# Performance work log

Measured on AMD Instinct MI355X. Metric: run time of the kernel, lower is better.

Reference implementation:

```python
import jax, jax.numpy as jnp
import numpy as np

Y_SCALE = 0.01  # fixed weight quantization scale (q_scale of the int8 weights)


def setup_inputs() -> dict:
    key = jax.random.key(0)
    kx, kw, kb = jax.random.split(key, 3)
    B, S, IN, OUT = 4, 2048, 4096, 4096
    x = jax.random.normal(kx, (B, S, IN), dtype=jnp.float32)
    # int8 quantized weights, stored transposed as (in_features, out_features)
    weight_q = jax.random.randint(kw, (IN, OUT), -128, 128, dtype=jnp.int32)
    bias = jax.random.normal(kb, (OUT,), dtype=jnp.float32)
    return {"x": x, "weight_q": weight_q, "bias": bias}


def reference(x, weight_q, bias):
    # Per-batch-sample dynamic activation scale: max(|x_i|)/128 over each [S, IN] slice
    x_scale = jnp.max(jnp.abs(x), axis=(1, 2), keepdims=True) / 128.0  # [B,1,1]
    # int8 quantize: round + clip
    xq = jnp.clip(jnp.round(x / x_scale), -128, 127).astype(jnp.int8)  # [B,S,IN]
    wq = weight_q.astype(jnp.int8)                                      # [IN,OUT]
    c = jax.lax.dot_general(
        xq, wq,
        dimension_numbers=(((2,), (0,)), ((), ())),
        preferred_element_type=jnp.int32,
    )  # [B,S,OUT]
    # dequantize and bias-add
    y = c.astype(jnp.float32) * (x_scale * Y_SCALE)
    return y + bias
```

## Files before the change

### kernel.cpp

```cpp
#include <hip/hip_runtime.h>
#include <stdint.h>

#define K_DIM 4096
#define N_DIM 4096
#define M_DIM 8192
#define S_ROWS 2048
#define NT 32

typedef int v4i __attribute__((ext_vector_type(4)));

__device__ __forceinline__ void gload16(const void* g, void* l) {
    __builtin_amdgcn_global_load_lds(
        (const __attribute__((address_space(1))) unsigned int*)g,
        (__attribute__((address_space(3))) unsigned int*)l, 16, 0, 0);
}

__device__ __forceinline__ void barrier() {
    asm volatile("" ::: "memory");
    __builtin_amdgcn_s_barrier();
    asm volatile("" ::: "memory");
}

__global__ void absmax_kernel(const float* __restrict__ x, unsigned* __restrict__ amax) {
    int b = blockIdx.y;
    const float4* xb = (const float4*)(x + (size_t)b * S_ROWS * K_DIM);
    int tid = blockIdx.x * 256 + threadIdx.x;
    const int stride = 1024 * 256;
    float m = 0.f;
#pragma unroll
    for (int i = 0; i < 8; ++i) {
        float4 v = xb[tid + i * stride];
        m = fmaxf(m, fmaxf(fmaxf(fabsf(v.x), fabsf(v.y)),
                           fmaxf(fabsf(v.z), fabsf(v.w))));
    }
#pragma unroll
    for (int off = 32; off; off >>= 1)
        m = fmaxf(m, __shfl_xor(m, off));
    __shared__ float red[4];
    if ((threadIdx.x & 63) == 0) red[threadIdx.x >> 6] = m;
    __syncthreads();
    if (threadIdx.x == 0) {
        m = fmaxf(fmaxf(red[0], red[1]), fmaxf(red[2], red[3]));
        atomicMax(&amax[b], __float_as_uint(m));
    }
}

__global__ void quant_kernel(const float* __restrict__ x,
                             const unsigned* __restrict__ amax,
                             char* __restrict__ xq) {
    size_t gid = (size_t)blockIdx.x * 256 + threadIdx.x;
    size_t base = gid * 16;
    int b = (int)(base >> 23);
    float inv = 128.0f / __uint_as_float(amax[b]);
    const float4* xs = (const float4*)(x + base);
    unsigned parts[4];
#pragma unroll
    for (int i = 0; i < 4; ++i) {
        float4 v = xs[i];
        int q0 = max(-128, min(127, (int)rintf(v.x * inv)));
        int q1 = max(-128, min(127, (int)rintf(v.y * inv)));
        int q2 = max(-128, min(127, (int)rintf(v.z * inv)));
        int q3 = max(-128, min(127, (int)rintf(v.w * inv)));
        parts[i] = (q0 & 255) | ((q1 & 255) << 8) | ((q2 & 255) << 16) | ((q3 & 255) << 24);
    }
    *(uint4*)(xq + base) = make_uint4(parts[0], parts[1], parts[2], parts[3]);
}

__global__ void wtrans_kernel(const int* __restrict__ wq, char* __restrict__ wt) {
    __shared__ unsigned lds[64 * 17];
    int t = threadIdx.x;
    int c = t & 63;
    int g = t >> 6;
    int n0 = blockIdx.x * 64;
    int k0 = blockIdx.y * 64;
#pragma unroll
    for (int rep = 0; rep < 4; ++rep) {
        int kb = g * 16 + rep * 4;
        int v0 = wq[(size_t)(k0 + kb + 0) * N_DIM + n0 + c];
        int v1 = wq[(size_t)(k0 + kb + 1) * N_DIM + n0 + c];
        int v2 = wq[(size_t)(k0 + kb + 2) * N_DIM + n0 + c];
        int v3 = wq[(size_t)(k0 + kb + 3) * N_DIM + n0 + c];
        lds[c * 17 + (kb >> 2)] =
            (v0 & 255) | ((v1 & 255) << 8) | ((v2 & 255) << 16) | ((v3 & 255) << 24);
    }
    __syncthreads();
    int row = t >> 2;
    int ch = t & 3;
    uint4 o;
    o.x = lds[row * 17 + ch * 4 + 0];
    o.y = lds[row * 17 + ch * 4 + 1];
    o.z = lds[row * 17 + ch * 4 + 2];
    o.w = lds[row * 17 + ch * 4 + 3];
    *(uint4*)(wt + (size_t)(n0 + row) * K_DIM + k0 + ch * 16) = o;
}

__global__ __launch_bounds__(512, 2) void gemm8_kernel(
    const char* __restrict__ A, const char* __restrict__ Bt,
    const float* __restrict__ bias, const unsigned* __restrict__ amax,
    float* __restrict__ out) {
    __shared__ char sm[131072];
    const int t = threadIdx.x;
    const int l = t & 63;
    const int w = t >> 6;
    const int wm = w >> 2;
    const int wn = w & 3;
    const int rb = l & 15;
    const int sg = l >> 4;

    int bid = blockIdx.x;
    int swz = (bid & 7) * 64 + (bid >> 3);
    int mt = swz >> 4, nt = swz & 15;
    const size_t m0 = (size_t)mt * 256;
    const size_t n0 = (size_t)nt * 256;

    v4i acc[8][4];
#pragma unroll
    for (int i = 0; i < 8; ++i)
#pragma unroll
        for (int j = 0; j < 4; ++j) acc[i][j] = (v4i){0, 0, 0, 0};

#define ST_A(tt, h)                                                          \
    if ((tt) < NT) {                                                         \
        char* lb = sm + (((tt) & 1) * 65536);                                \
        const char* gb = A + m0 * K_DIM + (size_t)(tt) * 128;                \
        _Pragma("unroll")                                                    \
        for (int j = 0; j < 2; ++j) {                                        \
            int p = j * 512 + t;                                             \
            int r7 = p >> 3, sl = p & 7;                                     \
            int r = (r7 & 63) + ((r7 >> 6) << 7) + ((h) << 6);               \
            int s = sl ^ (r & 7);                                            \
            gload16(gb + (size_t)r * K_DIM + s * 16, lb + r * 128 + sl * 16);\
        }                                                                    \
    }
#define ST_B(tt, h)                                                          \
    if ((tt) < NT) {                                                         \
        char* lb = sm + (((tt) & 1) * 65536) + 32768;                        \
        const char* gb = Bt + n0 * K_DIM + (size_t)(tt) * 128;               \
        _Pragma("unroll")                                                    \
        for (int j = 0; j < 2; ++j) {                                        \
            int p = j * 512 + t;                                             \
            int r7 = p >> 3, sl = p & 7;                                     \
            int r = ((r7 >> 5) << 6) + ((h) << 5) + (r7 & 31);               \
            int s = sl ^ (r & 7);                                            \
            gload16(gb + (size_t)r * K_DIM + s * 16, lb + r * 128 + sl * 16);\
        }                                                                    \
    }

    ST_A(0, 0); ST_B(0, 0); ST_A(0, 1); ST_B(0, 1); ST_A(1, 0); ST_B(1, 0);

    v4i aF[4][2], bF[4][2];

    for (int i = 0; i < NT; ++i) {
        const char* pA = sm + (i & 1) * 65536;
        const char* pB = pA + 32768;
        if (i == NT - 1) { asm volatile("s_waitcnt vmcnt(0)" ::: "memory"); }
        else             { asm volatile("s_waitcnt vmcnt(4)" ::: "memory"); }
        barrier();

#pragma unroll
        for (int mi = 0; mi < 4; ++mi)
#pragma unroll
            for (int ks = 0; ks < 2; ++ks) {
                int r = wm * 128 + mi * 16 + rb;
                aF[mi][ks] = *(const v4i*)(pA + r * 128 + (((ks << 2) + sg) ^ (r & 7)) * 16);
            }
#pragma unroll
        for (int ni = 0; ni < 2; ++ni)
#pragma unroll
            for (int ks = 0; ks < 2; ++ks) {
                int r = wn * 64 + ni * 16 + rb;
                bF[ni][ks] = *(const v4i*)(pB + r * 128 + (((ks << 2) + sg) ^ (r & 7)) * 16);
            }
        ST_A(i + 1, 1);
        barrier();
        asm volatile("s_waitcnt lgkmcnt(0)" ::: "memory");
        __builtin_amdgcn_s_setprio(1);
#pragma unroll
        for (int mi = 0; mi < 4; ++mi)
#pragma unroll
            for (int ni = 0; ni < 2; ++ni)
#pragma unroll
                for (int ks = 0; ks < 2; ++ks)
                    acc[mi][ni] = __builtin_amdgcn_mfma_i32_16x16x64_i8(
                        aF[mi][ks], bF[ni][ks], acc[mi][ni], 0, 0, 0);
        __builtin_amdgcn_s_setprio(0);
        barrier();

#pragma unroll
        for (int ni = 2; ni < 4; ++ni)
#pragma unroll
            for (int ks = 0; ks < 2; ++ks) {
                int r = wn * 64 + ni * 16 + rb;
                bF[ni][ks] = *(const v4i*)(pB + r * 128 + (((ks << 2) + sg) ^ (r & 7)) * 16);
            }
        ST_B(i + 1, 1);
        barrier();
        asm volatile("s_waitcnt lgkmcnt(0)" ::: "memory");
        __builtin_amdgcn_s_setprio(1);
#pragma unroll
        for (int mi = 0; mi < 4; ++mi)
#pragma unroll
            for (int ni = 2; ni < 4; ++ni)
#pragma unroll
                for (int ks = 0; ks < 2; ++ks)
                    acc[mi][ni] = __builtin_amdgcn_mfma_i32_16x16x64_i8(
                        aF[mi][ks], bF[ni][ks], acc[mi][ni], 0, 0, 0);
        __builtin_amdgcn_s_setprio(0);
        barrier();

#pragma unroll
        for (int mi = 0; mi < 4; ++mi)
#pragma unroll
            for (int ks = 0; ks < 2; ++ks) {
                int r = wm * 128 + 64 + mi * 16 + rb;
                aF[mi][ks] = *(const v4i*)(pA + r * 128 + (((ks << 2) + sg) ^ (r & 7)) * 16);
            }
        ST_A(i + 2, 0);
        barrier();
        asm volatile("s_waitcnt lgkmcnt(0)" ::: "memory");
        __builtin_amdgcn_s_setprio(1);
#pragma unroll
        for (int mi = 0; mi < 4; ++mi)
#pragma unroll
            for (int ni = 2; ni < 4; ++ni)
#pragma unroll
                for (int ks = 0; ks < 2; ++ks)
                    acc[mi + 4][ni] = __builtin_amdgcn_mfma_i32_16x16x64_i8(
                        aF[mi][ks], bF[ni][ks], acc[mi + 4][ni], 0, 0, 0);
        __builtin_amdgcn_s_setprio(0);
        barrier();

        ST_B(i + 2, 0);
        barrier();
        asm volatile("s_waitcnt lgkmcnt(0)" ::: "memory");
        __builtin_amdgcn_s_setprio(1);
#pragma unroll
        for (int mi = 0; mi < 4; ++mi)
#pragma unroll
            for (int ni = 0; ni < 2; ++ni)
#pragma unroll
                for (int ks = 0; ks < 2; ++ks)
                    acc[mi + 4][ni] = __builtin_amdgcn_mfma_i32_16x16x64_i8(
                        aF[mi][ks], bF[ni][ks], acc[mi + 4][ni], 0, 0, 0);
        __builtin_amdgcn_s_setprio(0);
        barrier();
    }

    float scale = __uint_as_float(amax[m0 >> 11]) * (1.0f / 128.0f) * 0.01f;
#pragma unroll
    for (int ni = 0; ni < 4; ++ni) {
        int col = (int)n0 + wn * 64 + ni * 16 + rb;
        float bv = bias[col];
#pragma unroll
        for (int mi = 0; mi < 8; ++mi) {
            size_t row = m0 + wm * 128 + mi * 16 + sg * 4;
#pragma unroll
            for (int rg = 0; rg < 4; ++rg)
                out[(row + rg) * N_DIM + col] = (float)acc[mi][ni][rg] * scale + bv;
        }
    }
#undef ST_A
#undef ST_B
}

extern "C" void kernel_launch(void* const* d_in, const int* in_sizes, int n_in,
                              void* d_out, int out_size, void* d_ws, size_t ws_size,
                              hipStream_t stream) {
    const float* x = (const float*)d_in[0];
    const int* wq = (const int*)d_in[1];
    const float* bias = (const float*)d_in[2];
    float* out = (float*)d_out;

    unsigned* amax = (unsigned*)d_ws;
    char* xq = (char*)d_ws + 256;
    char* wt = (char*)d_ws + 256 + (size_t)M_DIM * K_DIM;

    hipMemsetAsync(d_ws, 0, 16, stream);

    wtrans_kernel<<<dim3(64, 64), 256, 0, stream>>>(wq, wt);
    absmax_kernel<<<dim3(1024, 4), 256, 0, stream>>>(x, amax);
    quant_kernel<<<8192, 256, 0, stream>>>(x, amax, xq);
    gemm8_kernel<<<dim3(512), 512, 0, stream>>>(xq, wt, bias, amax, out);
}
```

Baseline: 236.4 us.

## Merge GEMM main-loop phases into two and drop redundant barriers and waits

Restructures the per-iteration schedule of the int8 MFMA GEMM from four load/compute phases to two. The full B tile for the current step is split into low and high register halves, and the next-stage A and B LDS prefetches are issued together. Several workgroup barriers and explicit lgkmcnt waits are removed, which should cut synchronisation stalls and let MFMA overlap more with LDS and global traffic. The epilogue is also reordered to hoist bias loads and walk output rows contiguously. The changes raise register pressure and depend on the remaining barriers still ordering buffer reuse correctly.

Measured after the change: 228.5 us. 3.3% less time.

```diff
diff --git a/kernel.cpp b/kernel.cpp
--- a/kernel.cpp
+++ b/kernel.cpp
@@ -148,7 +148,7 @@
 
     ST_A(0, 0); ST_B(0, 0); ST_A(0, 1); ST_B(0, 1); ST_A(1, 0); ST_B(1, 0);
 
-    v4i aF[4][2], bF[4][2];
+    v4i aF[4][2], bL[2][2], bH[2][2];
 
     for (int i = 0; i < NT; ++i) {
         const char* pA = sm + (i & 1) * 65536;
@@ -169,11 +169,10 @@
 #pragma unroll
             for (int ks = 0; ks < 2; ++ks) {
                 int r = wn * 64 + ni * 16 + rb;
-                bF[ni][ks] = *(const v4i*)(pB + r * 128 + (((ks << 2) + sg) ^ (r & 7)) * 16);
+                bL[ni][ks] = *(const v4i*)(pB + r * 128 + (((ks << 2) + sg) ^ (r & 7)) * 16);
             }
         ST_A(i + 1, 1);
-        barrier();
-        asm volatile("s_waitcnt lgkmcnt(0)" ::: "memory");
+        ST_B(i + 1, 1);
         __builtin_amdgcn_s_setprio(1);
 #pragma unroll
         for (int mi = 0; mi < 4; ++mi)
@@ -182,33 +181,26 @@
 #pragma unroll
                 for (int ks = 0; ks < 2; ++ks)
                     acc[mi][ni] = __builtin_amdgcn_mfma_i32_16x16x64_i8(
-                        aF[mi][ks], bF[ni][ks], acc[mi][ni], 0, 0, 0);
+                        aF[mi][ks], bL[ni][ks], acc[mi][ni], 0, 0, 0);
+#pragma unroll
+        for (int ni = 0; ni < 2; ++ni)
+#pragma unroll
+            for (int ks = 0; ks < 2; ++ks) {
+                int r = wn * 64 + 32 + ni * 16 + rb;
+                bH[ni][ks] = *(const v4i*)(pB + r * 128 + (((ks << 2) + sg) ^ (r & 7)) * 16);
+            }
+#pragma unroll
+        for (int mi = 0; mi < 4; ++mi)
+#pragma unroll
+            for (int ni = 0; ni < 2; ++ni)
+#pragma unroll
+                for (int ks = 0; ks < 2; ++ks)
+                    acc[mi][ni + 2] = __builtin_amdgcn_mfma_i32_16x16x64_i8(
+                        aF[mi][ks], bH[ni][ks], acc[mi][ni + 2], 0, 0, 0);
         __builtin_amdgcn_s_setprio(0);
         barrier();
 
 #pragma unroll
-        for (int ni = 2; ni < 4; ++ni)
-#pragma unroll
-            for (int ks = 0; ks < 2; ++ks) {
-                int r = wn * 64 + ni * 16 + rb;
-                bF[ni][ks] = *(const v4i*)(pB + r * 128 + (((ks << 2) + sg) ^ (r & 7)) * 16);
-            }
-        ST_B(i + 1, 1);
-        barrier();
-        asm volatile("s_waitcnt lgkmcnt(0)" ::: "memory");
-        __builtin_amdgcn_s_setprio(1);
-#pragma unroll
-        for (int mi = 0; mi < 4; ++mi)
-#pragma unroll
-            for (int ni = 2; ni < 4; ++ni)
-#pragma unroll
-                for (int ks = 0; ks < 2; ++ks)
-                    acc[mi][ni] = __builtin_amdgcn_mfma_i32_16x16x64_i8(
-                        aF[mi][ks], bF[ni][ks], acc[mi][ni], 0, 0, 0);
-        __builtin_amdgcn_s_setprio(0);
-        barrier();
-
-#pragma unroll
         for (int mi = 0; mi < 4; ++mi)
 #pragma unroll
             for (int ks = 0; ks < 2; ++ks) {
@@ -216,47 +208,40 @@
                 aF[mi][ks] = *(const v4i*)(pA + r * 128 + (((ks << 2) + sg) ^ (r & 7)) * 16);
             }
         ST_A(i + 2, 0);
-        barrier();
-        asm volatile("s_waitcnt lgkmcnt(0)" ::: "memory");
+        ST_B(i + 2, 0);
         __builtin_amdgcn_s_setprio(1);
 #pragma unroll
         for (int mi = 0; mi < 4; ++mi)
 #pragma unroll
-            for (int ni = 2; ni < 4; ++ni)
+            for (int ni = 0; ni < 2; ++ni)
+#pragma unroll
+                for (int ks = 0; ks < 2; ++ks)
+                    acc[mi + 4][ni + 2] = __builtin_amdgcn_mfma_i32_16x16x64_i8(
+                        aF[mi][ks], bH[ni][ks], acc[mi + 4][ni + 2], 0, 0, 0);
+#pragma unroll
+        for (int mi = 0; mi < 4; ++mi)
+#pragma unroll
+            for (int ni = 0; ni < 2; ++ni)
 #pragma unroll
                 for (int ks = 0; ks < 2; ++ks)
                     acc[mi + 4][ni] = __builtin_amdgcn_mfma_i32_16x16x64_i8(
-                        aF[mi][ks], bF[ni][ks], acc[mi + 4][ni], 0, 0, 0);
+                        aF[mi][ks], bL[ni][ks], acc[mi + 4][ni], 0, 0, 0);
         __builtin_amdgcn_s_setprio(0);
-        barrier();
-
-        ST_B(i + 2, 0);
-        barrier();
-        asm volatile("s_waitcnt lgkmcnt(0)" ::: "memory");
-        __builtin_amdgcn_s_setprio(1);
-#pragma unroll
-        for (int mi = 0; mi < 4; ++mi)
-#pragma unroll
-            for (int ni = 0; ni < 2; ++ni)
-#pragma unroll
-                for (int ks = 0; ks < 2; ++ks)
-                    acc[mi + 4][ni] = __builtin_amdgcn_mfma_i32_16x16x64_i8(
-                        aF[mi][ks], bF[ni][ks], acc[mi + 4][ni], 0, 0, 0);
-        __builtin_amdgcn_s_setprio(0);
-        barrier();
     }
 
     float scale = __uint_as_float(amax[m0 >> 11]) * (1.0f / 128.0f) * 0.01f;
-#pragma unroll
-    for (int ni = 0; ni < 4; ++ni) {
-        int col = (int)n0 + wn * 64 + ni * 16 + rb;
-        float bv = bias[col];
-#pragma unroll
-        for (int mi = 0; mi < 8; ++mi) {
-            size_t row = m0 + wm * 128 + mi * 16 + sg * 4;
-#pragma unroll
-            for (int rg = 0; rg < 4; ++rg)
-                out[(row + rg) * N_DIM + col] = (float)acc[mi][ni][rg] * scale + bv;
+    float bv[4];
+#pragma unroll
+    for (int ni = 0; ni < 4; ++ni) bv[ni] = bias[n0 + wn * 64 + ni * 16 + rb];
+#pragma unroll
+    for (int mi = 0; mi < 8; ++mi) {
+#pragma unroll
+        for (int rg = 0; rg < 4; ++rg) {
+            size_t row = m0 + wm * 128 + mi * 16 + sg * 4 + rg;
+            float* orow = out + row * N_DIM + n0 + wn * 64 + rb;
+#pragma unroll
+            for (int ni = 0; ni < 4; ++ni)
+                orow[ni * 16] = (float)acc[mi][ni][rg] * scale + bv[ni];
         }
     }
 #undef ST_A
```
